# Optimization experiments

Measured on AMD Instinct MI355X. Metric: run time of the kernel, lower is better.

The kernel has to match this reference:

```python
import jax, jax.numpy as jnp
import numpy as np

N_ITEMS = 30000
D = 128            # embedding_dim
F = D // 2 + 1     # freq_dim = 65
RAW_IMG = 1024
RAW_TXT = 768


def setup_inputs() -> dict:
    key = jax.random.key(0)
    ks = jax.random.split(key, 13)
    return {
        "image_embeds": jax.random.normal(ks[0], (N_ITEMS, D), jnp.float32),
        "text_embeds": jax.random.normal(ks[1], (N_ITEMS, D), jnp.float32),
        "image_table": jax.random.normal(ks[2], (N_ITEMS, RAW_IMG), jnp.float32),
        "text_table": jax.random.normal(ks[3], (N_ITEMS, RAW_TXT), jnp.float32),
        "W_img": jax.random.normal(ks[4], (RAW_IMG, D), jnp.float32) * 0.02,
        "b_img": jax.random.normal(ks[5], (D,), jnp.float32) * 0.02,
        "W_txt": jax.random.normal(ks[6], (RAW_TXT, D), jnp.float32) * 0.02,
        "b_txt": jax.random.normal(ks[7], (D,), jnp.float32) * 0.02,
        "avrf_img": jax.random.normal(ks[8], (F,), jnp.float32),
        "avrf_txt": jax.random.normal(ks[9], (F,), jnp.float32),
        "avg_R": jax.random.normal(ks[10], (F,), jnp.float32),
        "psi": jax.random.normal(ks[11], (F,), jnp.float32) * 0.1,
        "lambda_weights": jnp.array([0.6, 0.4], jnp.float32),
    }


def reference(image_embeds, text_embeds, image_table, text_table,
              W_img, b_img, W_txt, b_txt,
              avrf_img, avrf_txt, avg_R, psi, lambda_weights):
    # project full embedding tables: [N, raw] @ [raw, D] -> [N, D]
    proj_image = image_table @ W_img + b_img
    proj_txt = text_table @ W_txt + b_txt
    # per-row rFFT -> [N, F] complex
    img_fft = jnp.fft.rfft(proj_image, axis=1, norm="ortho")
    txt_fft = jnp.fft.rfft(proj_txt, axis=1, norm="ortho")
    # phase alignment rotation
    phi = avg_R * 0.5 + psi                      # [F]
    rot = jnp.exp(-1j * phi.astype(jnp.complex64))
    APC_img = img_fft * rot[None, :]
    APC_txt = txt_fft * jnp.conj(rot)[None, :]
    # AVRF (variance-ratio) masking -- torch forward uses the raw logit params
    img_vr = APC_img * avrf_img[None, :]
    txt_vr = APC_txt * avrf_txt[None, :]
    # IMCF: magnitude-squared coherence masking
    cross = APC_img * jnp.conj(APC_txt)
    msc = jnp.abs(cross) ** 2 / (jnp.abs(APC_img) ** 2 * jnp.abs(APC_txt) ** 2 + 1e-8)
    img_imcf = APC_img * msc
    txt_imcf = APC_txt * msc
    # softmax-weighted late fusion of the two filtered spectra
    lam = jax.nn.softmax(lambda_weights)
    img_late = lam[0] * img_vr + lam[1] * img_imcf
    txt_late = lam[0] * txt_vr + lam[1] * txt_imcf
    image_conv = jnp.fft.irfft(img_late, n=image_embeds.shape[1], axis=1, norm="ortho")
    text_conv = jnp.fft.irfft(txt_late, n=text_embeds.shape[1], axis=1, norm="ortho")
    return image_conv, text_conv
```

## Files before the change

kernel.cpp:

```cpp
#include <hip/hip_runtime.h>
#include <math.h>

typedef __bf16 bf16x8 __attribute__((ext_vector_type(8)));
typedef float f32x4 __attribute__((ext_vector_type(4)));
typedef unsigned short u16;
typedef unsigned int u32;

#define S128 0.08838834764831845f
#define TWOPI_128 0.04908738521234052f
#define MROWS 30016

__device__ __align__(16) u16 g_wft[56 * 12288];
__device__ __align__(16) u16 g_gt[6 * 8192];
__device__ __align__(16) float g_fp[96 * 8];
__device__ __align__(16) u32 g_S[(size_t)2 * 6 * 4 * MROWS * 8];

__device__ __forceinline__ void split2(float v, u16& h, u16& l) {
  unsigned u = __float_as_uint(v);
  h = (u16)(u >> 16);
  float hf = __uint_as_float(u & 0xFFFF0000u);
  float lo = v - hf;
  unsigned ul = __float_as_uint(lo);
  l = (u16)((ul + 0x7FFFu + ((ul >> 16) & 1u)) >> 16);
}

__device__ __forceinline__ void gll16(const void* gsrc, void* ldst) {
  __builtin_amdgcn_global_load_lds(
      (const __attribute__((address_space(1))) unsigned int*)gsrc,
      (__attribute__((address_space(3))) unsigned int*)ldst, 16, 0, 0);
}

__global__ void k_setup_wft(const float* __restrict__ Wimg,
                            const float* __restrict__ Wtxt, int Kimg, int Ktxt) {
  int gid = blockIdx.x * 256 + threadIdx.x;
  int imgn = Kimg * 96;
  if (gid >= imgn + Ktxt * 96) return;
  const float* Wrow;
  u16* base;
  int kloc, fq;
  if (gid < imgn) {
    kloc = gid / 96; fq = gid % 96;
    Wrow = Wimg + (size_t)kloc * 128;
    base = g_wft + (size_t)(kloc >> 5) * 12288;
  } else {
    int l = gid - imgn;
    kloc = l / 96; fq = l % 96;
    Wrow = Wtxt + (size_t)kloc * 128;
    base = g_wft + (size_t)(32 + (kloc >> 5)) * 12288;
  }
  float re = 0.f, im = 0.f;
  if (fq <= 64) {
    float sts, stc;
    sincosf(TWOPI_128 * (float)fq, &sts, &stc);
    for (int d0 = 0; d0 < 128; d0 += 16) {
      int m = (fq * d0) & 127;
      float sa, ca;
      sincosf(TWOPI_128 * (float)m, &sa, &ca);
      float cr = ca, ci = -sa;
      float wv[16];
      *(float4*)&wv[0]  = *(const float4*)&Wrow[d0];
      *(float4*)&wv[4]  = *(const float4*)&Wrow[d0 + 4];
      *(float4*)&wv[8]  = *(const float4*)&Wrow[d0 + 8];
      *(float4*)&wv[12] = *(const float4*)&Wrow[d0 + 12];
#pragma unroll
      for (int jj = 0; jj < 16; ++jj) {
        re = fmaf(wv[jj], cr, re);
        im = fmaf(wv[jj], ci, im);
        float nc = cr * stc + ci * sts;
        ci = ci * stc - cr * sts;
        cr = nc;
      }
    }
    re *= S128; im *= S128;
  }
  int gran = (kloc & 31) >> 3, j = kloc & 7;
  int cre = (fq >> 4) * 32 + (fq & 15);
  u16 h, l;
  split2(re, h, l);
  base[(gran * 1536 + cre * 8 + j) ^ (gran << 4)] = h;
  base[6144 + ((gran * 1536 + cre * 8 + j) ^ (gran << 4))] = l;
  split2(im, h, l);
  base[(gran * 1536 + (cre + 16) * 8 + j) ^ (gran << 4)] = h;
  base[6144 + ((gran * 1536 + (cre + 16) * 8 + j) ^ (gran << 4))] = l;
}

__global__ void k_setup_gt(void) {
  int gid = blockIdx.x * 256 + threadIdx.x;
  if (gid >= 192 * 128) return;
  int pk = gid >> 7, n = gid & 127;
  int ks = pk >> 5, w = pk & 31, gran = (w >> 3) & 3, j = w & 7;
  int part = w >> 4, fl = ks * 16 + (w & 15);
  float val = 0.f;
  if (fl <= 64) {
    float ck = (fl == 0 || fl == 64) ? 1.f : 2.f;
    int m = (fl * n) & 127;
    float sa, ca;
    sincosf(TWOPI_128 * (float)m, &sa, &ca);
    val = (part == 0 ? ca : -sa) * ck * S128;
  }
  u16 h, l;
  split2(val, h, l);
  g_gt[ks * 8192 + ((gran * 1024 + n * 8 + j) ^ (gran << 4))] = h;
  g_gt[ks * 8192 + 4096 + ((gran * 1024 + n * 8 + j) ^ (gran << 4))] = l;
}

__global__ void k_setup_fp(const float* __restrict__ b_img, const float* __restrict__ b_txt,
                           const float* __restrict__ avrf_img, const float* __restrict__ avrf_txt,
                           const float* __restrict__ avg_R, const float* __restrict__ psi) {
  int gid = blockIdx.x * 256 + threadIdx.x;
  if (gid >= 96 * 4) return;
  int k = gid >> 2, q = gid & 3;
  float* fp = g_fp + k * 8;
  if (k > 64) {
    if (q == 0) { fp[0] = 1.f; fp[1] = 0.f; fp[2] = 0.f; fp[3] = 0.f; }
    fp[4 + q] = 0.f;
    return;
  }
  if (q == 0) {
    float phi = avg_R[k] * 0.5f + psi[k];
    float s, c;
    sincosf(phi, &s, &c);
    fp[0] = c; fp[1] = s; fp[2] = avrf_img[k]; fp[3] = avrf_txt[k];
  }
  const float* b = (q < 2) ? b_img : b_txt;
  int part = q & 1;
  float acc = 0.f;
  for (int d = 0; d < 128; ++d) {
    int m = (k * d) & 127;
    float sa, ca;
    sincosf(TWOPI_128 * (float)m, &sa, &ca);
    acc = fmaf(b[d], part ? -sa : ca, acc);
  }
  fp[4 + q] = acc * S128;
}

__global__ __launch_bounds__(256) void k1_gemm(
    const float* __restrict__ Aimg, const float* __restrict__ Atxt,
    int M, int Kimg, int Ktxt, int bpm) {
  __shared__ __align__(16) u16 Asm[4096];
  __shared__ __align__(16) u16 Bsm[2 * 12288];

  const int bid = blockIdx.x;
  const int mod = bid >= bpm;
  const int bblk = mod ? bid - bpm : bid;
  const float* A = mod ? Atxt : Aimg;
  const int K = mod ? Ktxt : Kimg;
  const u16* wft = g_wft + (mod ? (size_t)32 * 12288 : 0);
  const int row0 = bblk * 64;

  const int tid = threadIdx.x;
  const int lane = tid & 63, wv = tid >> 6;
  const int la = lane & 15, hh = lane >> 4;
  const int wr = wv >> 1, wc = wv & 1;

  const int rseg = tid >> 2, g4 = tid & 3;
  const int awoff = (g4 * 512 + rseg * 8) ^ (g4 << 4);
  int grow = row0 + rseg;
  if (grow > M - 1) grow = M - 1;
  const float* Abase = A + (size_t)grow * K + g4 * 8;

  f32x4 acc[2][6];
#pragma unroll
  for (int rt = 0; rt < 2; ++rt)
#pragma unroll
    for (int ct = 0; ct < 6; ++ct) acc[rt][ct] = (f32x4){0.f, 0.f, 0.f, 0.f};

  const int nst = K / 32;

  auto stageB = [&](int s, int buf) {
    const u16* src = wft + (size_t)s * 12288;
    char* dst = (char*)Bsm + buf * 24576;
#pragma unroll
    for (int i = 0; i < 6; ++i)
      gll16(src + i * 2048 + tid * 8, dst + i * 4096 + tid * 16);
  };

  stageB(0, 0);
  float4 av0 = *(const float4*)(Abase);
  float4 av1 = *(const float4*)(Abase + 4);

  for (int s = 0; s < nst; ++s) {
    const int cur = s & 1;
    __syncthreads();
    {
      u16 h8[8], l8[8];
      const float va[8] = {av0.x, av0.y, av0.z, av0.w, av1.x, av1.y, av1.z, av1.w};
#pragma unroll
      for (int j = 0; j < 8; ++j) split2(va[j], h8[j], l8[j]);
      *(bf16x8*)&Asm[awoff] = *(bf16x8*)h8;
      *(bf16x8*)&Asm[2048 + awoff] = *(bf16x8*)l8;
    }
    __syncthreads();

    if (s + 1 < nst) {
      stageB(s + 1, cur ^ 1);
      av0 = *(const float4*)(Abase + (s + 1) * 32);
      av1 = *(const float4*)(Abase + (s + 1) * 32 + 4);
    }

    bf16x8 fah[2], fal[2];
#pragma unroll
    for (int rt = 0; rt < 2; ++rt) {
      const int ar = wr * 32 + rt * 16 + la;
      const int off = (hh * 512 + ar * 8) ^ (hh << 4);
      fah[rt] = *(const bf16x8*)&Asm[off];
      fal[rt] = *(const bf16x8*)&Asm[2048 + off];
    }
#pragma unroll
    for (int ct = 0; ct < 6; ++ct) {
      const int col = wc * 96 + ct * 16 + la;
      const u16* bb = &Bsm[cur * 12288 + ((hh * 1536 + col * 8) ^ (hh << 4))];
      const bf16x8 fbh = *(const bf16x8*)bb;
      const bf16x8 fbl = *(const bf16x8*)(bb + 6144);
#pragma unroll
      for (int rt = 0; rt < 2; ++rt) {
        acc[rt][ct] = __builtin_amdgcn_mfma_f32_16x16x32_bf16(fah[rt], fbh, acc[rt][ct], 0, 0, 0);
        acc[rt][ct] = __builtin_amdgcn_mfma_f32_16x16x32_bf16(fah[rt], fbl, acc[rt][ct], 0, 0, 0);
        acc[rt][ct] = __builtin_amdgcn_mfma_f32_16x16x32_bf16(fal[rt], fbh, acc[rt][ct], 0, 0, 0);
      }
    }
  }

#pragma unroll
  for (int ct = 0; ct < 6; ++ct) {
    const int cg = wc * 6 + ct;
    const int fq = (cg >> 1) * 16 + la;
    const float bv = g_fp[fq * 8 + 4 + mod * 2 + (cg & 1)];
    const int ks = cg >> 1;
    const int khh = (cg & 1) * 2 + (la >> 3);
    const int j8 = la & 7;
    const size_t sbase = ((size_t)((mod * 6 + ks) * 4 + khh)) * MROWS;
#pragma unroll
    for (int rt = 0; rt < 2; ++rt) {
      const int rb = row0 + wr * 32 + rt * 16 + hh * 4;
#pragma unroll
      for (int j = 0; j < 4; ++j) {
        u16 h, l;
        split2(acc[rt][ct][j] + bv, h, l);
        g_S[(sbase + rb + j) * 8 + j8] = ((u32)h << 16) | l;
      }
    }
  }
}

__global__ __launch_bounds__(256) void k2_idft(
    const float* __restrict__ lamw, float* __restrict__ out, int M) {
  __shared__ __align__(16) u16 Gs[8192];
  __shared__ __align__(16) float fps[96 * 8];

  const int tid = threadIdx.x;
  const int lane = tid & 63, wv = tid >> 6;
  const int la = lane & 15, hh = lane >> 4;
  const int part = hh >> 1;
  const int row = blockIdx.x * 64 + wv * 16 + la;

  if (tid < 192) gll16((const char*)g_fp + tid * 16, (char*)fps + tid * 16);

  const float l0 = lamw[0], l1 = lamw[1];
  const float mx = fmaxf(l0, l1);
  const float e0 = expf(l0 - mx), e1 = expf(l1 - mx);
  const float lam0 = e0 / (e0 + e1), lam1 = e1 / (e0 + e1);

  f32x4 ai[8], at[8];
#pragma unroll
  for (int ct = 0; ct < 8; ++ct) {
    ai[ct] = (f32x4){0.f, 0.f, 0.f, 0.f};
    at[ct] = (f32x4){0.f, 0.f, 0.f, 0.f};
  }

  for (int ks = 0; ks < 6; ++ks) {
    const u32* si = &g_S[((size_t)((0 + ks) * 4 + hh) * MROWS + row) * 8];
    const u32* st = &g_S[((size_t)((24 + ks * 4) + hh) * MROWS + row) * 8];
    uint4 vi0 = *(const uint4*)si, vi1 = *(const uint4*)(si + 4);
    uint4 vt0 = *(const uint4*)st, vt1 = *(const uint4*)(st + 4);

    __syncthreads();
#pragma unroll
    for (int i = 0; i < 4; ++i)
      gll16((const char*)(g_gt + ks * 8192) + i * 4096 + tid * 16,
            (char*)Gs + i * 4096 + tid * 16);
    __syncthreads();

    u32 vs_i[8], vs_t[8];
    *(uint4*)&vs_i[0] = vi0; *(uint4*)&vs_i[4] = vi1;
    *(uint4*)&vs_t[0] = vt0; *(uint4*)&vs_t[4] = vt1;

    const int fq0 = ks * 16 + (hh & 1) * 8;
    u16 yih[8], yil[8], yth[8], ytl[8];
#pragma unroll
    for (int j = 0; j < 8; ++j) {
      const f32x4 fpv = *(const f32x4*)&fps[(fq0 + j) * 8];
      const float o_i = __uint_as_float(vs_i[j] & 0xFFFF0000u) + __uint_as_float(vs_i[j] << 16);
      const float o_t = __uint_as_float(vs_t[j] & 0xFFFF0000u) + __uint_as_float(vs_t[j] << 16);
      const float p_i = __shfl_xor(o_i, 32);
      const float p_t = __shfl_xor(o_t, 32);
      const float Sre_i = part ? p_i : o_i;
      const float Sim_i = part ? o_i : p_i;
      const float Sre_t = part ? p_t : o_t;
      const float Sim_t = part ? o_t : p_t;
      const float rc = fpv[0], rs = fpv[1];
      const float Air = Sre_i * rc + Sim_i * rs, Aii = Sim_i * rc - Sre_i * rs;
      const float Atr = Sre_t * rc - Sim_t * rs, Ati = Sim_t * rc + Sre_t * rs;
      const float cre = Air * Atr + Aii * Ati, cim = Aii * Atr - Air * Ati;
      const float pa = Air * Air + Aii * Aii, pb = Atr * Atr + Ati * Ati;
      const float msc = (cre * cre + cim * cim) / (pa * pb + 1e-8f);
      const float mi = lam0 * fpv[2] + lam1 * msc;
      const float mt = lam0 * fpv[3] + lam1 * msc;
      const float yi = (part ? Aii : Air) * mi;
      const float yt = (part ? Ati : Atr) * mt;
      split2(yi, yih[j], yil[j]);
      split2(yt, yth[j], ytl[j]);
    }
    const bf16x8 fih = *(bf16x8*)yih, fil = *(bf16x8*)yil;
    const bf16x8 fth = *(bf16x8*)yth, ftl = *(bf16x8*)ytl;
#pragma unroll
    for (int ct = 0; ct < 8; ++ct) {
      const int goff = (hh * 1024 + (ct * 16 + la) * 8) ^ (hh << 4);
      const bf16x8 gh = *(const bf16x8*)&Gs[goff];
      const bf16x8 gl = *(const bf16x8*)&Gs[4096 + goff];
      ai[ct] = __builtin_amdgcn_mfma_f32_16x16x32_bf16(fih, gh, ai[ct], 0, 0, 0);
      ai[ct] = __builtin_amdgcn_mfma_f32_16x16x32_bf16(fih, gl, ai[ct], 0, 0, 0);
      ai[ct] = __builtin_amdgcn_mfma_f32_16x16x32_bf16(fil, gh, ai[ct], 0, 0, 0);
      at[ct] = __builtin_amdgcn_mfma_f32_16x16x32_bf16(fth, gh, at[ct], 0, 0, 0);
      at[ct] = __builtin_amdgcn_mfma_f32_16x16x32_bf16(fth, gl, at[ct], 0, 0, 0);
      at[ct] = __builtin_amdgcn_mfma_f32_16x16x32_bf16(ftl, gh, at[ct], 0, 0, 0);
    }
  }

  float* oimg = out;
  float* otxt = out + (size_t)M * 128;
#pragma unroll
  for (int q = 0; q < 4; ++q) {
    const int orow = blockIdx.x * 64 + wv * 16 + hh * 4 + q;
    if (orow < M) {
#pragma unroll
      for (int ct = 0; ct < 8; ++ct) {
        oimg[(size_t)orow * 128 + ct * 16 + la] = ai[ct][q];
        otxt[(size_t)orow * 128 + ct * 16 + la] = at[ct][q];
      }
    }
  }
}

extern "C" void kernel_launch(void* const* d_in, const int* in_sizes, int n_in,
                              void* d_out, int out_size, void* d_ws, size_t ws_size,
                              hipStream_t stream) {
  const float* image_table = (const float*)d_in[2];
  const float* text_table  = (const float*)d_in[3];
  const float* W_img = (const float*)d_in[4];
  const float* b_img = (const float*)d_in[5];
  const float* W_txt = (const float*)d_in[6];
  const float* b_txt = (const float*)d_in[7];
  const float* avrf_img = (const float*)d_in[8];
  const float* avrf_txt = (const float*)d_in[9];
  const float* avg_R = (const float*)d_in[10];
  const float* psi = (const float*)d_in[11];
  const float* lamw = (const float*)d_in[12];

  const int M = in_sizes[0] / 128;
  const int K_img = in_sizes[4] / 128;
  const int K_txt = in_sizes[6] / 128;

  const int wft_threads = (K_img + K_txt) * 96;
  k_setup_wft<<<(wft_threads + 255) / 256, 256, 0, stream>>>(W_img, W_txt, K_img, K_txt);
  k_setup_gt<<<(192 * 128 + 255) / 256, 256, 0, stream>>>();
  k_setup_fp<<<2, 256, 0, stream>>>(b_img, b_txt, avrf_img, avrf_txt, avg_R, psi);

  const int bpm = (M + 63) / 64;
  k1_gemm<<<2 * bpm, 256, 0, stream>>>(image_table, text_table, M, K_img, K_txt, bpm);
  k2_idft<<<bpm, 256, 0, stream>>>(lamw, (float*)d_out, M);
}
```

Measured before the change: 159.7 us.

## Load GEMM operands directly into registers, dropping LDS staging and barriers

```diff
diff --git a/kernel.cpp b/kernel.cpp
--- a/kernel.cpp
+++ b/kernel.cpp
@@ -137,9 +137,6 @@
 __global__ __launch_bounds__(256) void k1_gemm(
     const float* __restrict__ Aimg, const float* __restrict__ Atxt,
     int M, int Kimg, int Ktxt, int bpm) {
-  __shared__ __align__(16) u16 Asm[4096];
-  __shared__ __align__(16) u16 Bsm[2 * 12288];
-
   const int bid = blockIdx.x;
   const int mod = bid >= bpm;
   const int bblk = mod ? bid - bpm : bid;
@@ -153,11 +150,10 @@
   const int la = lane & 15, hh = lane >> 4;
   const int wr = wv >> 1, wc = wv & 1;
 
-  const int rseg = tid >> 2, g4 = tid & 3;
-  const int awoff = (g4 * 512 + rseg * 8) ^ (g4 << 4);
-  int grow = row0 + rseg;
-  if (grow > M - 1) grow = M - 1;
-  const float* Abase = A + (size_t)grow * K + g4 * 8;
+  int r0 = row0 + wr * 32 + la;      if (r0 > M - 1) r0 = M - 1;
+  int r1 = row0 + wr * 32 + 16 + la; if (r1 > M - 1) r1 = M - 1;
+  const float* Ar0 = A + (size_t)r0 * K + hh * 8;
+  const float* Ar1 = A + (size_t)r1 * K + hh * 8;
 
   f32x4 acc[2][6];
 #pragma unroll
@@ -165,53 +161,48 @@
 #pragma unroll
     for (int ct = 0; ct < 6; ++ct) acc[rt][ct] = (f32x4){0.f, 0.f, 0.f, 0.f};
 
+  int boff[6];
+#pragma unroll
+  for (int ct = 0; ct < 6; ++ct)
+    boff[ct] = (hh * 1536 + (wc * 96 + ct * 16 + la) * 8) ^ (hh << 4);
+
   const int nst = K / 32;
 
-  auto stageB = [&](int s, int buf) {
-    const u16* src = wft + (size_t)s * 12288;
-    char* dst = (char*)Bsm + buf * 24576;
-#pragma unroll
-    for (int i = 0; i < 6; ++i)
-      gll16(src + i * 2048 + tid * 8, dst + i * 4096 + tid * 16);
-  };
-
-  stageB(0, 0);
-  float4 av0 = *(const float4*)(Abase);
-  float4 av1 = *(const float4*)(Abase + 4);
-
+  float4 av0 = *(const float4*)(Ar0);
+  float4 av1 = *(const float4*)(Ar0 + 4);
+  float4 av2 = *(const float4*)(Ar1);
+  float4 av3 = *(const float4*)(Ar1 + 4);
+
+  const u16* bch = wft;
   for (int s = 0; s < nst; ++s) {
-    const int cur = s & 1;
-    __syncthreads();
+    bf16x8 fah[2], fal[2];
     {
       u16 h8[8], l8[8];
-      const float va[8] = {av0.x, av0.y, av0.z, av0.w, av1.x, av1.y, av1.z, av1.w};
-#pragma unroll
-      for (int j = 0; j < 8; ++j) split2(va[j], h8[j], l8[j]);
-      *(bf16x8*)&Asm[awoff] = *(bf16x8*)h8;
-      *(bf16x8*)&Asm[2048 + awoff] = *(bf16x8*)l8;
-    }
-    __syncthreads();
-
+#pragma unroll
+      for (int j = 0; j < 4; ++j) {
+        split2(av0[j], h8[j], l8[j]);
+        split2(av1[j], h8[4 + j], l8[4 + j]);
+      }
+      fah[0] = *(bf16x8*)h8; fal[0] = *(bf16x8*)l8;
+#pragma unroll
+      for (int j = 0; j < 4; ++j) {
+        split2(av2[j], h8[j], l8[j]);
+        split2(av3[j], h8[4 + j], l8[4 + j]);
+      }
+      fah[1] = *(bf16x8*)h8; fal[1] = *(bf16x8*)l8;
+    }
     if (s + 1 < nst) {
-      stageB(s + 1, cur ^ 1);
-      av0 = *(const float4*)(Abase + (s + 1) * 32);
-      av1 = *(const float4*)(Abase + (s + 1) * 32 + 4);
-    }
-
-    bf16x8 fah[2], fal[2];
-#pragma unroll
-    for (int rt = 0; rt < 2; ++rt) {
-      const int ar = wr * 32 + rt * 16 + la;
-      const int off = (hh * 512 + ar * 8) ^ (hh << 4);
-      fah[rt] = *(const bf16x8*)&Asm[off];
-      fal[rt] = *(const bf16x8*)&Asm[2048 + off];
+      const float* p0 = Ar0 + (s + 1) * 32;
+      const float* p1 = Ar1 + (s + 1) * 32;
+      av0 = *(const float4*)(p0);
+      av1 = *(const float4*)(p0 + 4);
+      av2 = *(const float4*)(p1);
+      av3 = *(const float4*)(p1 + 4);
     }
 #pragma unroll
     for (int ct = 0; ct < 6; ++ct) {
-      const int col = wc * 96 + ct * 16 + la;
-      const u16* bb = &Bsm[cur * 12288 + ((hh * 1536 + col * 8) ^ (hh << 4))];
-      const bf16x8 fbh = *(const bf16x8*)bb;
-      const bf16x8 fbl = *(const bf16x8*)(bb + 6144);
+      const bf16x8 fbh = *(const bf16x8*)&bch[boff[ct]];
+      const bf16x8 fbl = *(const bf16x8*)&bch[6144 + boff[ct]];
 #pragma unroll
       for (int rt = 0; rt < 2; ++rt) {
         acc[rt][ct] = __builtin_amdgcn_mfma_f32_16x16x32_bf16(fah[rt], fbh, acc[rt][ct], 0, 0, 0);
@@ -219,6 +210,7 @@
         acc[rt][ct] = __builtin_amdgcn_mfma_f32_16x16x32_bf16(fal[rt], fbh, acc[rt][ct], 0, 0, 0);
       }
     }
+    bch += 12288;
   }
 
 #pragma unroll
```

Measured after the change: 233.3 us. 1.46x slower.
